# Kernel optimization log

Hardware: AMD Instinct MI355X
Metric: run time of the kernel (lower is better)

The kernel has to match this reference:

```python
import jax, jax.numpy as jnp
import numpy as np

N_SERIES = 2048
N_TIME = 4096
INPUT_SIZE = 28
OUTPUT_SIZE = 7
SEASONALITY = 7                      # single seasonal period (weekly)
EMBEDS_SIZE = 1 + 1 + SEASONALITY    # lev_sm logit, seas_sm logit, log init seasons


def setup_inputs() -> dict:
    key = jax.random.key(0)
    k1, k2 = jax.random.split(key)
    # strictly positive series (divided and log-ed in normalize)
    y = jax.random.uniform(k1, (N_SERIES, N_TIME), dtype=jnp.float32) + 0.5
    idxs = jnp.arange(N_SERIES, dtype=jnp.int32)
    embeds_weight = 0.5 + 0.1 * jax.random.normal(k2, (N_SERIES, EMBEDS_SIZE), dtype=jnp.float32)
    return {"y": y, "idxs": idxs, "embeds_weight": embeds_weight}


def _compute_levels_seasons(y, idxs, embeds_weight):
    embeds = embeds_weight[idxs]                        # (B, 9)
    lev_sms = jax.nn.sigmoid(embeds[:, 0])              # (B,)
    seas_sms = jax.nn.sigmoid(embeds[:, 1])             # (B,)
    init_seas = jnp.exp(embeds[:, 2:2 + SEASONALITY])   # (B, m)

    level0 = y[:, 0] / init_seas[:, 0]                  # (B,)
    # torch builds seasonalities1 = [s0..s_{m-1}, s0]; step t (t>=1) reads index t
    # and appends index m+t. Equivalent ring buffer ordered by next-read:
    buf0 = jnp.concatenate([init_seas[:, 1:], init_seas[:, :1]], axis=1)  # (B, m)

    def step(carry, y_t):
        level, buf = carry
        season_t = buf[:, 0]
        newlev = lev_sms * (y_t / season_t) + (1.0 - lev_sms) * level
        newseason = seas_sms * (y_t / newlev) + (1.0 - seas_sms) * season_t
        buf = jnp.concatenate([buf[:, 1:], newseason[:, None]], axis=1)
        return (newlev, buf), (newlev, newseason)

    (_, _), (levs, seas) = jax.lax.scan(step, (level0, buf0), y[:, 1:].T)
    levels = jnp.concatenate([level0[:, None], levs.T], axis=1)          # (B, T)
    init_list = jnp.concatenate([init_seas, init_seas[:, :1]], axis=1)   # (B, m+1)
    seasonalities = jnp.concatenate([init_list, seas.T], axis=1)         # (B, T+m)
    return levels, seasonalities


def reference(y, idxs, embeds_weight):
    levels, seasonalities = _compute_levels_seasons(y, idxs, embeds_weight)
    n_time = y.shape[1]
    # eval-mode windows: range(n_time - I - O + 1, n_time - I + 1) -> O windows
    windows_start = n_time - INPUT_SIZE - OUTPUT_SIZE + 1
    n_windows = OUTPUT_SIZE
    starts = windows_start + jnp.arange(n_windows)                  # (W,)
    t_idx = starts[:, None] + jnp.arange(INPUT_SIZE)[None, :]       # (W, I)
    y_win = y[:, t_idx]                                             # (B, W, I)
    seas_win = seasonalities[:, t_idx]                              # (B, W, I)
    lev_win = levels[:, starts + INPUT_SIZE - 1]                    # (B, W)
    # normalize: log(y / level / season)
    windows_y_hat = jnp.log(y_win / lev_win[:, :, None] / seas_win)
    windows_y_hat = jnp.transpose(windows_y_hat, (1, 0, 2))         # (W, B, I)
    windows_y = jnp.zeros((n_windows, y.shape[0], OUTPUT_SIZE), dtype=y.dtype)
    return windows_y_hat, windows_y, levels, seasonalities
```

## Files before the change

kernel.cpp:

```cpp
#include <hip/hip_runtime.h>

#define N_SERIES 2048
#define N_TIME   4096
#define SEAS     7
#define EMB      9
#define INPUT_SIZE 28
#define OUTPUT_SIZE 7

#define OUT0_N (OUTPUT_SIZE * N_SERIES * INPUT_SIZE)
#define OUT1_N (OUTPUT_SIZE * N_SERIES * OUTPUT_SIZE)
#define LEV_N  (N_SERIES * N_TIME)
#define SEA_N  (N_SERIES * (N_TIME + SEAS))

#define LCH  112
#define WUP  224
#define NCH  37
#define TT   56
#define PADS 65
#define WSP  (NCH * N_SERIES)

__device__ __forceinline__ float rcp_(float x){ return __builtin_amdgcn_rcpf(x); }
__device__ __forceinline__ float log2_(float x){ return __builtin_amdgcn_logf(x); }

__global__ __launch_bounds__(64) void es_stageA(
    const float* __restrict__ y, const int* __restrict__ idxs,
    const float* __restrict__ emb, float* __restrict__ ws)
{
    __shared__ float ly[TT][PADS];
    const int lane = threadIdx.x;
    const int c = blockIdx.x % NCH, g = blockIdx.x / NCH;
    const int s0 = g * 64, s = s0 + lane;
    const int t0 = 1 + c * LCH;
    const bool exact = (c <= 2);
    const int tw = exact ? 1 : (t0 - WUP);
    const int ntiles = (c == 0) ? 2 : ((c == 1) ? 4 : 6);
    const int save_tt = (c == 1) ? 1 : 3;

    const float* e = emb + (size_t)idxs[s] * EMB;
    const float lev_sms  = 1.f / (1.f + expf(-e[0]));
    const float seas_sms = 1.f / (1.f + expf(-e[1]));
    const float oml = 1.f - lev_sms, oms = 1.f - seas_sms;

    float ring[7], rsl[7], level;
    if (exact) {
        float einit[7];
#pragma unroll
        for (int j = 0; j < 7; ++j) einit[j] = expf(e[2 + j]);
#pragma unroll
        for (int j = 0; j < 7; ++j) ring[j] = einit[(1 + j) % 7];
        level = y[(size_t)s * N_TIME] * rcp_(einit[0]);
    } else {
#pragma unroll
        for (int j = 0; j < 7; ++j) ring[j] = 1.64872127f;
        level = y[(size_t)s * N_TIME + (tw - 1)] * 0.60653066f;
    }
#pragma unroll
    for (int j = 0; j < 7; ++j) rsl[j] = lev_sms * rcp_(ring[j]);

    float svlev = 1.f, svring[7];
#pragma unroll
    for (int j = 0; j < 7; ++j) svring[j] = 1.f;

    for (int tt = 0; tt < ntiles; ++tt) {
        const int tb = tw + tt * TT;
#pragma unroll 8
        for (int r = 0; r < 64; ++r) {
            if (lane < TT) {
                int t = tb + lane; if (t > N_TIME - 1) t = N_TIME - 1;
                ly[lane][r] = y[(size_t)(s0 + r) * N_TIME + t];
            }
        }
        for (int g8 = 0; g8 < 8; ++g8) {
#pragma unroll
            for (int j = 0; j < 7; ++j) {
                const int k = g8 * 7 + j;
                float yt = ly[k][lane];
                float nl = fmaf(oml, level, yt * rsl[j]);
                float rl = rcp_(nl);
                float ns = fmaf(oms, ring[j], (seas_sms * yt) * rl);
                ring[j] = ns;
                rsl[j]  = lev_sms * rcp_(ns);
                level = nl;
            }
        }
        if (c != 0 && tt == save_tt) {
            svlev = level;
#pragma unroll
            for (int j = 0; j < 7; ++j) svring[j] = ring[j];
        }
    }

    float A = 0.f;
#pragma unroll
    for (int j = 0; j < 7; ++j) A += log2_(ring[j]);
    ws[8 * WSP + c * N_SERIES + s] = A;
    if (c != 0) {
        float B = 0.f;
#pragma unroll
        for (int j = 0; j < 7; ++j) B += log2_(svring[j]);
        ws[9 * WSP + c * N_SERIES + s] = B;
        ws[0 * WSP + c * N_SERIES + s] = svlev;
#pragma unroll
        for (int j = 0; j < 7; ++j)
            ws[(1 + j) * WSP + c * N_SERIES + s] = svring[j];
    }
}

__global__ __launch_bounds__(64) void es_chain(float* __restrict__ ws)
{
    const int s = blockIdx.x * 64 + threadIdx.x;
    float kap = 0.f;
    ws[10 * WSP + 0 * N_SERIES + s] = 0.f;
    float Aprev = ws[8 * WSP + 0 * N_SERIES + s];
    for (int c = 1; c < NCH; ++c) {
        float B = ws[9 * WSP + c * N_SERIES + s];
        kap += (Aprev - B) * (1.f / 7.f);
        ws[10 * WSP + c * N_SERIES + s] = kap;
        Aprev = ws[8 * WSP + c * N_SERIES + s];
    }
}

__global__ __launch_bounds__(64) void es_stageC(
    const float* __restrict__ y, const int* __restrict__ idxs,
    const float* __restrict__ emb, const float* __restrict__ ws,
    float* __restrict__ levels, float* __restrict__ seas_out)
{
    __shared__ float ly[TT][PADS], llev[TT][PADS], lsea[TT][PADS];
    const int lane = threadIdx.x;
    const int c = blockIdx.x % NCH, g = blockIdx.x / NCH;
    const int s0 = g * 64, s = s0 + lane;
    const int t0 = 1 + c * LCH;

    const float* e = emb + (size_t)idxs[s] * EMB;
    const float lev_sms  = 1.f / (1.f + expf(-e[0]));
    const float seas_sms = 1.f / (1.f + expf(-e[1]));
    const float oml = 1.f - lev_sms, oms = 1.f - seas_sms;

    float ring[7], rsl[7], level;
    if (c == 0) {
        float einit[7];
#pragma unroll
        for (int j = 0; j < 7; ++j) einit[j] = expf(e[2 + j]);
#pragma unroll
        for (int j = 0; j < 7; ++j) ring[j] = einit[(1 + j) % 7];
        level = y[(size_t)s * N_TIME] * rcp_(einit[0]);
        levels[(size_t)s * N_TIME] = level;
        float* sr = seas_out + (size_t)s * (N_TIME + SEAS);
#pragma unroll
        for (int j = 0; j < 7; ++j) sr[j] = einit[j];
        sr[7] = einit[0];
    } else {
        float kap = ws[10 * WSP + c * N_SERIES + s];
        float f  = exp2f(kap);
        float fi = exp2f(-kap);
        level = ws[0 * WSP + c * N_SERIES + s] * fi;
#pragma unroll
        for (int j = 0; j < 7; ++j)
            ring[j] = ws[(1 + j) * WSP + c * N_SERIES + s] * f;
    }
#pragma unroll
    for (int j = 0; j < 7; ++j) rsl[j] = lev_sms * rcp_(ring[j]);

    for (int tt = 0; tt < 2; ++tt) {
        const int tb = t0 + tt * TT;
#pragma unroll 8
        for (int r = 0; r < 64; ++r) {
            if (lane < TT) {
                int t = tb + lane; if (t > N_TIME - 1) t = N_TIME - 1;
                ly[lane][r] = y[(size_t)(s0 + r) * N_TIME + t];
            }
        }
        for (int g8 = 0; g8 < 8; ++g8) {
#pragma unroll
            for (int j = 0; j < 7; ++j) {
                const int k = g8 * 7 + j;
                float yt = ly[k][lane];
                float nl = fmaf(oml, level, yt * rsl[j]);
                float rl = rcp_(nl);
                float ns = fmaf(oms, ring[j], (seas_sms * yt) * rl);
                ring[j] = ns;
                rsl[j]  = lev_sms * rcp_(ns);
                llev[k][lane] = nl;
                lsea[k][lane] = ns;
                level = nl;
            }
        }
        if (lane < TT) {
            const int t = tb + lane;
            if (t <= N_TIME - 1) {
#pragma unroll 8
                for (int r = 0; r < 64; ++r) {
                    levels[(size_t)(s0 + r) * N_TIME + t] = llev[lane][r];
                    seas_out[(size_t)(s0 + r) * (N_TIME + SEAS) + SEAS + t] = lsea[lane][r];
                }
            }
        }
    }
}

__global__ __launch_bounds__(256) void es_windows(
    const float* __restrict__ y,
    const float* __restrict__ levels,
    const float* __restrict__ seas,
    float* __restrict__ out0,
    float* __restrict__ out1)
{
    int tid = blockIdx.x * 256 + threadIdx.x;
    if (tid < OUT0_N) {
        int i = tid % INPUT_SIZE;
        int r = tid / INPUT_SIZE;
        int s = r & (N_SERIES - 1);
        int w = r >> 11;
        int t = (N_TIME - INPUT_SIZE - OUTPUT_SIZE + 1) + w + i;
        float yt = y[(size_t)s * N_TIME + t];
        float lv = levels[(size_t)s * N_TIME + (N_TIME - OUTPUT_SIZE + w)];
        float sv = seas[(size_t)s * (N_TIME + SEAS) + t];
        float ratio = yt * rcp_(lv * sv);
        out0[tid] = log2_(ratio) * 0.6931471805599453f;
    } else {
        int j = tid - OUT0_N;
        if (j < OUT1_N) out1[j] = 0.0f;
    }
}

extern "C" void kernel_launch(void* const* d_in, const int* in_sizes, int n_in,
                              void* d_out, int out_size, void* d_ws, size_t ws_size,
                              hipStream_t stream) {
    const float* y    = (const float*)d_in[0];
    const int*   idxs = (const int*)d_in[1];
    const float* emb  = (const float*)d_in[2];

    float* out  = (float*)d_out;
    float* out0 = out;
    float* out1 = out + OUT0_N;
    float* lev  = out + OUT0_N + OUT1_N;
    float* sea  = out + OUT0_N + OUT1_N + LEV_N;
    float* ws   = (float*)d_ws;

    es_stageA<<<32 * NCH, 64, 0, stream>>>(y, idxs, emb, ws);
    es_chain<<<N_SERIES / 64, 64, 0, stream>>>(ws);
    es_stageC<<<32 * NCH, 64, 0, stream>>>(y, idxs, emb, ws, lev, sea);
    es_windows<<<(OUT0_N + OUT1_N) / 256, 256, 0, stream>>>(y, lev, sea, out0, out1);
}
```

Baseline: 159.9 us.

## Double-buffer y tiles via async global_load_lds and move out1 zeroing to chain kernel

Replaces the synchronous register-staged loads of y into LDS with async global_load_lds, so the next tile's loads overlap the current tile's recurrence in stage A and stage C. The LDS layout becomes series-major, so each lane reads its own row, and stage C writes out through a transposed layout. It also moves the zero-fill of out1 into the chain kernel using float4 stores and shrinks the windows grid. The gamble is that the load_lds wave-wide write pattern matches the row-per-series layout; LDS footprint grows and correctness depends on the lane-to-address mapping of global_load_lds.

```diff
diff --git a/kernel.cpp b/kernel.cpp
--- a/kernel.cpp
+++ b/kernel.cpp
@@ -16,17 +16,33 @@
 #define WUP  224
 #define NCH  37
 #define TT   56
-#define PADS 65
+#define STR  65
 #define WSP  (NCH * N_SERIES)
 
 __device__ __forceinline__ float rcp_(float x){ return __builtin_amdgcn_rcpf(x); }
 __device__ __forceinline__ float log2_(float x){ return __builtin_amdgcn_logf(x); }
+
+#define GLD_LDS(gp, lp)                                                        \
+    __builtin_amdgcn_global_load_lds(                                          \
+        (const __attribute__((address_space(1))) unsigned int*)(gp),           \
+        (__attribute__((address_space(3))) unsigned int*)(lp), 4, 0, 0)
+
+#define WAIT_VM0() asm volatile("s_waitcnt vmcnt(0)" ::: "memory")
+
+__device__ __forceinline__ void stage_tile(
+    const float* __restrict__ y, int s0, int tb, int lane, float (*lbuf)[STR])
+{
+    int t = tb + lane; t = (t > N_TIME - 1) ? (N_TIME - 1) : t;
+#pragma unroll 16
+    for (int r = 0; r < 64; ++r)
+        GLD_LDS(&y[(size_t)(s0 + r) * N_TIME + t], &lbuf[r][0]);
+}
 
 __global__ __launch_bounds__(64) void es_stageA(
     const float* __restrict__ y, const int* __restrict__ idxs,
     const float* __restrict__ emb, float* __restrict__ ws)
 {
-    __shared__ float ly[TT][PADS];
+    __shared__ float ly[2][64][STR];
     const int lane = threadIdx.x;
     const int c = blockIdx.x % NCH, g = blockIdx.x / NCH;
     const int s0 = g * 64, s = s0 + lane;
@@ -36,6 +52,8 @@
     const int ntiles = (c == 0) ? 2 : ((c == 1) ? 4 : 6);
     const int save_tt = (c == 1) ? 1 : 3;
 
+    stage_tile(y, s0, tw, lane, ly[0]);
+
     const float* e = emb + (size_t)idxs[s] * EMB;
     const float lev_sms  = 1.f / (1.f + expf(-e[0]));
     const float seas_sms = 1.f / (1.f + expf(-e[1]));
@@ -61,20 +79,17 @@
 #pragma unroll
     for (int j = 0; j < 7; ++j) svring[j] = 1.f;
 
+    WAIT_VM0();
     for (int tt = 0; tt < ntiles; ++tt) {
-        const int tb = tw + tt * TT;
-#pragma unroll 8
-        for (int r = 0; r < 64; ++r) {
-            if (lane < TT) {
-                int t = tb + lane; if (t > N_TIME - 1) t = N_TIME - 1;
-                ly[lane][r] = y[(size_t)(s0 + r) * N_TIME + t];
-            }
-        }
+        const int cur = tt & 1;
+        if (tt + 1 < ntiles)
+            stage_tile(y, s0, tw + (tt + 1) * TT, lane, ly[cur ^ 1]);
+        const float* yrow = &ly[cur][lane][0];
         for (int g8 = 0; g8 < 8; ++g8) {
 #pragma unroll
             for (int j = 0; j < 7; ++j) {
                 const int k = g8 * 7 + j;
-                float yt = ly[k][lane];
+                float yt = yrow[k];
                 float nl = fmaf(oml, level, yt * rsl[j]);
                 float rl = rcp_(nl);
                 float ns = fmaf(oms, ring[j], (seas_sms * yt) * rl);
@@ -88,6 +103,7 @@
 #pragma unroll
             for (int j = 0; j < 7; ++j) svring[j] = ring[j];
         }
+        WAIT_VM0();
     }
 
     float A = 0.f;
@@ -106,9 +122,15 @@
     }
 }
 
-__global__ __launch_bounds__(64) void es_chain(float* __restrict__ ws)
-{
-    const int s = blockIdx.x * 64 + threadIdx.x;
+__global__ __launch_bounds__(64) void es_chain(float* __restrict__ ws,
+                                               float* __restrict__ out1)
+{
+    const int tid = blockIdx.x * 64 + threadIdx.x;
+    float4 z4 = {0.f, 0.f, 0.f, 0.f};
+    for (int i = tid; i < OUT1_N / 4; i += N_SERIES)
+        ((float4*)out1)[i] = z4;
+
+    const int s = tid;
     float kap = 0.f;
     ws[10 * WSP + 0 * N_SERIES + s] = 0.f;
     float Aprev = ws[8 * WSP + 0 * N_SERIES + s];
@@ -125,11 +147,13 @@
     const float* __restrict__ emb, const float* __restrict__ ws,
     float* __restrict__ levels, float* __restrict__ seas_out)
 {
-    __shared__ float ly[TT][PADS], llev[TT][PADS], lsea[TT][PADS];
+    __shared__ float ly[64][STR], llev[64][STR], lsea[64][STR];
     const int lane = threadIdx.x;
     const int c = blockIdx.x % NCH, g = blockIdx.x / NCH;
     const int s0 = g * 64, s = s0 + lane;
     const int t0 = 1 + c * LCH;
+
+    stage_tile(y, s0, t0, lane, ly);
 
     const float* e = emb + (size_t)idxs[s] * EMB;
     const float lev_sms  = 1.f / (1.f + expf(-e[0]));
@@ -163,35 +187,34 @@
 
     for (int tt = 0; tt < 2; ++tt) {
         const int tb = t0 + tt * TT;
-#pragma unroll 8
-        for (int r = 0; r < 64; ++r) {
-            if (lane < TT) {
-                int t = tb + lane; if (t > N_TIME - 1) t = N_TIME - 1;
-                ly[lane][r] = y[(size_t)(s0 + r) * N_TIME + t];
-            }
-        }
+        WAIT_VM0();
+        const float* yrow = &ly[lane][0];
+        float* lrow = &llev[lane][0];
+        float* srow = &lsea[lane][0];
         for (int g8 = 0; g8 < 8; ++g8) {
 #pragma unroll
             for (int j = 0; j < 7; ++j) {
                 const int k = g8 * 7 + j;
-                float yt = ly[k][lane];
+                float yt = yrow[k];
                 float nl = fmaf(oml, level, yt * rsl[j]);
                 float rl = rcp_(nl);
                 float ns = fmaf(oms, ring[j], (seas_sms * yt) * rl);
                 ring[j] = ns;
                 rsl[j]  = lev_sms * rcp_(ns);
-                llev[k][lane] = nl;
-                lsea[k][lane] = ns;
+                lrow[k] = nl;
+                srow[k] = ns;
                 level = nl;
             }
         }
+        if (tt == 0)
+            stage_tile(y, s0, t0 + TT, lane, ly);
         if (lane < TT) {
             const int t = tb + lane;
             if (t <= N_TIME - 1) {
 #pragma unroll 8
                 for (int r = 0; r < 64; ++r) {
-                    levels[(size_t)(s0 + r) * N_TIME + t] = llev[lane][r];
-                    seas_out[(size_t)(s0 + r) * (N_TIME + SEAS) + SEAS + t] = lsea[lane][r];
+                    levels[(size_t)(s0 + r) * N_TIME + t] = llev[r][lane];
+                    seas_out[(size_t)(s0 + r) * (N_TIME + SEAS) + SEAS + t] = lsea[r][lane];
                 }
             }
         }
@@ -202,25 +225,19 @@
     const float* __restrict__ y,
     const float* __restrict__ levels,
     const float* __restrict__ seas,
-    float* __restrict__ out0,
-    float* __restrict__ out1)
+    float* __restrict__ out0)
 {
     int tid = blockIdx.x * 256 + threadIdx.x;
-    if (tid < OUT0_N) {
-        int i = tid % INPUT_SIZE;
-        int r = tid / INPUT_SIZE;
-        int s = r & (N_SERIES - 1);
-        int w = r >> 11;
-        int t = (N_TIME - INPUT_SIZE - OUTPUT_SIZE + 1) + w + i;
-        float yt = y[(size_t)s * N_TIME + t];
-        float lv = levels[(size_t)s * N_TIME + (N_TIME - OUTPUT_SIZE + w)];
-        float sv = seas[(size_t)s * (N_TIME + SEAS) + t];
-        float ratio = yt * rcp_(lv * sv);
-        out0[tid] = log2_(ratio) * 0.6931471805599453f;
-    } else {
-        int j = tid - OUT0_N;
-        if (j < OUT1_N) out1[j] = 0.0f;
-    }
+    int i = tid % INPUT_SIZE;
+    int r = tid / INPUT_SIZE;
+    int s = r & (N_SERIES - 1);
+    int w = r >> 11;
+    int t = (N_TIME - INPUT_SIZE - OUTPUT_SIZE + 1) + w + i;
+    float yt = y[(size_t)s * N_TIME + t];
+    float lv = levels[(size_t)s * N_TIME + (N_TIME - OUTPUT_SIZE + w)];
+    float sv = seas[(size_t)s * (N_TIME + SEAS) + t];
+    float ratio = yt * rcp_(lv * sv);
+    out0[tid] = log2_(ratio) * 0.6931471805599453f;
 }
 
 extern "C" void kernel_launch(void* const* d_in, const int* in_sizes, int n_in,
@@ -238,7 +255,7 @@
     float* ws   = (float*)d_ws;
 
     es_stageA<<<32 * NCH, 64, 0, stream>>>(y, idxs, emb, ws);
-    es_chain<<<N_SERIES / 64, 64, 0, stream>>>(ws);
+    es_chain<<<N_SERIES / 64, 64, 0, stream>>>(ws, out1);
     es_stageC<<<32 * NCH, 64, 0, stream>>>(y, idxs, emb, ws, lev, sea);
-    es_windows<<<(OUT0_N + OUT1_N) / 256, 256, 0, stream>>>(y, lev, sea, out0, out1);
-}
+    es_windows<<<OUT0_N / 256, 256, 0, stream>>>(y, lev, sea, out0);
+}
```

Measured after the change: 142.5 us. 1.12x faster.
